# Kernel tuning notes

Measured on AMD Instinct MI355X. Metric: run time of the kernel, lower is better.

The kernel has to match this reference:

```python
import jax, jax.numpy as jnp
import numpy as np
import math

B, S, D, H = 2, 4096, 768, 12
HD = D // H  # head_dim = 64


def setup_inputs() -> dict:
    key = jax.random.key(0)
    ks = jax.random.split(key, 12)
    scale = 1.0 / math.sqrt(D)
    inp = {
        "query": jax.random.normal(ks[0], (B, S, D), jnp.float32),
        "key_": jax.random.normal(ks[1], (B, S, D), jnp.float32),
        "value": jax.random.normal(ks[2], (B, S, D), jnp.float32),
        # causal mask: masked_fill where mask == 0
        "mask": jnp.tril(jnp.ones((S, S), jnp.int32))[None, None, :, :],
        "Wq": jax.random.normal(ks[3], (D, D), jnp.float32) * scale,
        "bq": jax.random.normal(ks[4], (D,), jnp.float32) * scale,
        "Wk": jax.random.normal(ks[5], (D, D), jnp.float32) * scale,
        "bk": jax.random.normal(ks[6], (D,), jnp.float32) * scale,
        "Wv": jax.random.normal(ks[7], (D, D), jnp.float32) * scale,
        "bv": jax.random.normal(ks[8], (D,), jnp.float32) * scale,
        "Wo": jax.random.normal(ks[9], (D, D), jnp.float32) * scale,
        "bo": jax.random.normal(ks[10], (D,), jnp.float32) * scale,
    }
    return inp


def reference(query, key_, value, mask, Wq, bq, Wk, bk, Wv, bv, Wo, bo):
    b, s, d = query.shape
    # Linear: x @ W.T + b (torch convention), split heads -> [B, H, S, HD]
    q = (query @ Wq.T + bq).reshape(b, s, H, HD).transpose(0, 2, 1, 3)
    k = (key_ @ Wk.T + bk).reshape(b, s, H, HD).transpose(0, 2, 1, 3)
    v = (value @ Wv.T + bv).reshape(b, s, H, HD).transpose(0, 2, 1, 3)
    # explicit [B, H, S, S] scores as in the source module
    scores = jnp.einsum("bhqd,bhkd->bhqk", q, k) / math.sqrt(HD)
    scores = jnp.where(mask == 0, -jnp.inf, scores)
    attn = jax.nn.softmax(scores, axis=-1)  # dropout p=0.0 -> identity
    out = jnp.einsum("bhqk,bhkd->bhqd", attn, v)
    out = out.transpose(0, 2, 1, 3).reshape(b, s, d)
    return out @ Wo.T + bo
```

## Files before the change

kernel.cpp:

```cpp
#include <hip/hip_runtime.h>

#define Sq 4096
#define Dm 768
#define Hh 12
#define KD 768

typedef short short8 __attribute__((ext_vector_type(8)));
typedef float f32x4 __attribute__((ext_vector_type(4)));
typedef unsigned short bf_t;

__device__ inline bf_t f2bf(float f) {
    unsigned int u = __builtin_bit_cast(unsigned int, f);
    u += 0x7fffu + ((u >> 16) & 1u);
    return (bf_t)(u >> 16);
}

__device__ inline unsigned int pk2bf(float a, float b) {
    unsigned int ua = __builtin_bit_cast(unsigned int, a) + 0x8000u;
    unsigned int ub = __builtin_bit_cast(unsigned int, b) + 0x8000u;
    return __builtin_amdgcn_perm(ub, ua, 0x07060302);
}

__device__ inline float fexp2(float x) {
#if __has_builtin(__builtin_amdgcn_exp2f)
    return __builtin_amdgcn_exp2f(x);
#else
    return exp2f(x);
#endif
}

__device__ inline void gl_lds16(const void* g, void* l) {
    __builtin_amdgcn_global_load_lds(
        (const __attribute__((address_space(1))) unsigned int*)g,
        (__attribute__((address_space(3))) unsigned int*)l, 16, 0, 0);
}

struct CvtJobs { const float* s[8]; bf_t* d[8]; int n[8]; };

__global__ __launch_bounds__(256) void cvt(CvtJobs jobs) {
    const float* s = jobs.s[blockIdx.z];
    bf_t* d = jobs.d[blockIdx.z];
    int n = jobs.n[blockIdx.z];
    int i = (blockIdx.x * 256 + threadIdx.x) * 8;
    if (i < n) {
        float4 a = *(const float4*)(s + i);
        float4 b = *(const float4*)(s + i + 4);
        short8 p;
        p[0] = (short)f2bf(a.x); p[1] = (short)f2bf(a.y);
        p[2] = (short)f2bf(a.z); p[3] = (short)f2bf(a.w);
        p[4] = (short)f2bf(b.x); p[5] = (short)f2bf(b.y);
        p[6] = (short)f2bf(b.z); p[7] = (short)f2bf(b.w);
        *(short8*)(d + i) = p;
    }
}

struct GemmJob {
    const bf_t* __restrict__ A; const bf_t* __restrict__ Bm;
    const float* __restrict__ bias; void* __restrict__ out;
    int mode; float scale;
};
struct GemmJobs { GemmJob j[3]; };

__global__ __launch_bounds__(256) void gemm_k(GemmJobs jobs) {
    const GemmJob J = jobs.j[blockIdx.z];
    __shared__ bf_t As[128 * 64];
    __shared__ bf_t Bs[128 * 64];
    const int lane = threadIdx.x & 63, wv = threadIdx.x >> 6;
    const int l16 = lane & 15, quad = lane >> 4;
    const int wm = wv >> 1, wn = wv & 1;
    int m0, n0;
    if (J.mode == 1) { m0 = blockIdx.y * 128; n0 = blockIdx.x * 128; }
    else             { m0 = blockIdx.x * 128; n0 = blockIdx.y * 128; }

    f32x4 acc[4][4] = {};

    for (int kk = 0; kk < KD; kk += 64) {
#pragma unroll
        for (int it = 0; it < 4; ++it) {
            int p0 = it * 256 + wv * 64;
            int p = p0 + lane;
            int row = p >> 3;
            int c = (p & 7) ^ (row & 7);
            gl_lds16(J.A + (size_t)(m0 + row) * KD + kk + c * 8, As + p0 * 8);
            gl_lds16(J.Bm + (size_t)(n0 + row) * KD + kk + c * 8, Bs + p0 * 8);
        }
        __syncthreads();
#pragma unroll
        for (int ks = 0; ks < 2; ++ks) {
            short8 a[4], b[4];
#pragma unroll
            for (int i = 0; i < 4; ++i) {
                int row = wm * 64 + i * 16 + l16;
                int pc = (ks * 4 + quad) ^ (row & 7);
                a[i] = *(const short8*)&As[row * 64 + pc * 8];
            }
#pragma unroll
            for (int j = 0; j < 4; ++j) {
                int row = wn * 64 + j * 16 + l16;
                int pc = (ks * 4 + quad) ^ (row & 7);
                b[j] = *(const short8*)&Bs[row * 64 + pc * 8];
            }
#pragma unroll
            for (int i = 0; i < 4; ++i)
#pragma unroll
                for (int j = 0; j < 4; ++j)
                    acc[i][j] = __builtin_amdgcn_mfma_f32_16x16x32_bf16(a[i], b[j], acc[i][j], 0, 0, 0);
        }
        __syncthreads();
    }

#pragma unroll
    for (int i = 0; i < 4; ++i) {
#pragma unroll
        for (int j = 0; j < 4; ++j) {
            int grow = m0 + wm * 64 + i * 16 + quad * 4;
            int gcol = n0 + wn * 64 + j * 16 + l16;
            if (J.mode == 0) {
                float bv = J.bias[gcol];
                int h = gcol >> 6, hd = gcol & 63;
                bf_t* dst = (bf_t*)J.out;
#pragma unroll
                for (int r = 0; r < 4; ++r) {
                    int row = grow + r;
                    int bI = row >> 12, s = row & 4095;
                    dst[(((size_t)(bI * Hh + h) * Sq + s) << 6) + hd] =
                        f2bf((acc[i][j][r] + bv) * J.scale);
                }
            } else if (J.mode == 3) {
                float bv = J.bias[gcol];
                int hh = gcol >> 6, hd = gcol & 63;
                int h2 = hd >> 5, rem = hd & 31, qd = rem >> 3, j2 = rem & 7;
                bf_t* dst = (bf_t*)J.out;
#pragma unroll
                for (int r = 0; r < 4; ++r) {
                    int row = grow + r;
                    int bI = row >> 12, s = row & 4095;
                    int kt2 = s >> 6, rr = s & 63;
                    int g2 = rr >> 5, r5 = rr & 31;
                    int a2 = r5 >> 3, s22 = (r5 >> 2) & 1, b2 = r5 & 3;
                    int lane2 = qd * 16 + (4 * a2 + b2);
                    dst[(size_t)(bI * Hh + hh) * Sq * 64 +
                        kt2 * 4096 + (2 * g2 + s22) * 1024 + h2 * 512 + lane2 * 8 + j2] =
                        f2bf(acc[i][j][r] + bv);
                }
            } else if (J.mode == 1) {
                bf_t* dst = (bf_t*)J.out;
                int t = gcol, bI = t >> 12, s = t & 4095;
                int kt2 = s >> 6, rr = s & 63;
                int g2 = rr >> 5, qd = (rr & 31) >> 3, j2 = rr & 7;
#pragma unroll
                for (int r = 0; r < 4; ++r) {
                    int f = grow + r;
                    int hh = f >> 6, hd = f & 63;
                    int ot = hd >> 4, l16v = hd & 15;
                    int lane2 = qd * 16 + l16v;
                    dst[(size_t)(bI * Hh + hh) * Sq * 64 +
                        kt2 * 4096 + (g2 * 4 + ot) * 512 + lane2 * 8 + j2] =
                        f2bf(acc[i][j][r] + J.bias[f]);
                }
            } else {
                float bv = J.bias[gcol];
                float* dst = (float*)J.out;
#pragma unroll
                for (int r = 0; r < 4; ++r)
                    dst[(size_t)(grow + r) * Dm + gcol] = acc[i][j][r] + bv;
            }
        }
    }
}

#define SHIFT 18.0f
#define NQ 4

__global__ __launch_bounds__(256) void attn(const bf_t* __restrict__ Q,
                                            const bf_t* __restrict__ K,
                                            const bf_t* __restrict__ VT,
                                            bf_t* __restrict__ O) {
    const int id = blockIdx.x + 24 * blockIdx.y;
    const int xcd = id & 7, slot = id >> 3;
    const int bh = xcd * 3 + slot % 3;
    const int qt = 31 - slot / 3;
    const int lane = threadIdx.x & 63, wv = threadIdx.x >> 6;
    const int rg = wv & 1, ksp = wv >> 1;
    const int l16 = lane & 15, quad = lane >> 4;
    const int b = bh / Hh, h = bh % Hh;
    const size_t base = (size_t)bh * Sq * 64;
    const int q0 = qt * 128 + rg * 64;

    __shared__ float ocomb[2][64][68];
    __shared__ float lcomb[2][64];

    const bf_t* __restrict__ Kb = K + base;
    const bf_t* __restrict__ Vb = VT + base;

    short8 qf[NQ][2];
#pragma unroll
    for (int i = 0; i < NQ; ++i) {
        const bf_t* qp = Q + base + (size_t)(q0 + i * 16 + l16) * 64 + quad * 8;
        qf[i][0] = *(const short8*)qp;
        qf[i][1] = *(const short8*)(qp + 32);
    }

    f32x4 oacc[NQ][4] = {};
    f32x4 lsum[NQ] = {};

    const int nkt = (q0 >> 6) + 1;
    const int hsp = (nkt + 1) >> 1;
    const int kt0 = ksp ? hsp : 0;
    const int kt1 = ksp ? nkt : hsp;

    short8 ones32;
#pragma unroll
    for (int j = 0; j < 8; ++j) ones32[j] = (short)0x3F80;

    short8 kf[4][2];
    short8 vfr[4][2];

    int ko = kt0 * 4096 + lane * 8;
    int vo = kt0 * 4096 + lane * 8;

#define LOAD_K()                                                             \
    {                                                                        \
        _Pragma("unroll")                                                    \
        for (int t = 0; t < 4; ++t) {                                        \
            kf[t][0] = *(const short8*)(Kb + ko + t * 1024);                 \
            kf[t][1] = *(const short8*)(Kb + ko + t * 1024 + 512);           \
        }                                                                    \
    }
#define LOAD_V()                                                             \
    {                                                                        \
        _Pragma("unroll")                                                    \
        for (int ot = 0; ot < 4; ++ot)                                       \
            _Pragma("unroll")                                                \
            for (int g = 0; g < 2; ++g)                                      \
                vfr[ot][g] = *(const short8*)(Vb + vo + (g * 4 + ot) * 512); \
    }

    if (kt0 < kt1) { LOAD_K(); LOAD_V(); }

    for (int kt = kt0; kt < kt1; ++kt) {
        const int kv0 = kt * 64;
        const bool more = (kt + 1 < kt1);
#pragma unroll
        for (int i = 0; i < NQ; ++i) {
            f32x4 st[4];
#pragma unroll
            for (int t = 0; t < 4; ++t) {
                f32x4 z = {-SHIFT, -SHIFT, -SHIFT, -SHIFT};
                z = __builtin_amdgcn_mfma_f32_16x16x32_bf16(kf[t][0], qf[i][0], z, 0, 0, 0);
                st[t] = __builtin_amdgcn_mfma_f32_16x16x32_bf16(kf[t][1], qf[i][1], z, 0, 0, 0);
            }
            if (i == NQ - 1) { ko += 4096; if (more) LOAD_K(); }

            alignas(16) unsigned int pkd[4][2];
            const bool need_mask = (kv0 + 63 > q0 + i * 16);
#pragma unroll
            for (int t = 0; t < 4; ++t) {
                int g = t >> 1, s = t & 1;
                f32x4 sv = st[t];
                if (need_mask) {
                    int qrow = q0 + i * 16 + l16;
                    int kb2 = kv0 + 32 * g + 8 * quad + 4 * s;
#pragma unroll
                    for (int r = 0; r < 4; ++r)
                        if (kb2 + r > qrow) sv[r] = -1e30f;
                }
                pkd[t][0] = pk2bf(fexp2(sv[0]), fexp2(sv[1]));
                pkd[t][1] = pk2bf(fexp2(sv[2]), fexp2(sv[3]));
            }
#pragma unroll
            for (int g = 0; g < 2; ++g) {
                short8 pf = *(const short8*)&pkd[2 * g][0];
                lsum[i] = __builtin_amdgcn_mfma_f32_16x16x32_bf16(ones32, pf, lsum[i], 0, 0, 0);
#pragma unroll
                for (int ot = 0; ot < 4; ++ot)
                    oacc[i][ot] = __builtin_amdgcn_mfma_f32_16x16x32_bf16(vfr[ot][g], pf, oacc[i][ot], 0, 0, 0);
            }
        }
        vo += 4096;
        if (more) LOAD_V();
    }
#undef LOAD_K
#undef LOAD_V

    if (ksp) {
#pragma unroll
        for (int i = 0; i < NQ; ++i) {
            int row = i * 16 + l16;
#pragma unroll
            for (int ot = 0; ot < 4; ++ot)
                *(f32x4*)&ocomb[rg][row][ot * 16 + quad * 4] = oacc[i][ot];
            if (quad == 0) lcomb[rg][row] = lsum[i][0];
        }
    }
    __syncthreads();
    if (!ksp) {
#pragma unroll
        for (int i = 0; i < NQ; ++i) {
            int row = i * 16 + l16;
            float ls = lsum[i][0] + lcomb[rg][row];
            float inv = 1.0f / ls;
            int srow = q0 + row;
            bf_t* orow = O + (size_t)(b * Sq + srow) * Dm + h * 64;
#pragma unroll
            for (int ot = 0; ot < 4; ++ot) {
                f32x4 oc = *(const f32x4*)&ocomb[rg][row][ot * 16 + quad * 4];
                uint2 pk;
                pk.x = pk2bf((oacc[i][ot][0] + oc[0]) * inv, (oacc[i][ot][1] + oc[1]) * inv);
                pk.y = pk2bf((oacc[i][ot][2] + oc[2]) * inv, (oacc[i][ot][3] + oc[3]) * inv);
                *(uint2*)(orow + ot * 16 + quad * 4) = pk;
            }
        }
    }
}

extern "C" void kernel_launch(void* const* d_in, const int* in_sizes, int n_in,
                              void* d_out, int out_size, void* d_ws, size_t ws_size,
                              hipStream_t stream) {
    const float* q  = (const float*)d_in[0];
    const float* k  = (const float*)d_in[1];
    const float* v  = (const float*)d_in[2];
    const float* Wq = (const float*)d_in[4];  const float* bq = (const float*)d_in[5];
    const float* Wk = (const float*)d_in[6];  const float* bk = (const float*)d_in[7];
    const float* Wv = (const float*)d_in[8];  const float* bv = (const float*)d_in[9];
    const float* Wo = (const float*)d_in[10]; const float* bo = (const float*)d_in[11];
    float* out = (float*)d_out;

    const float QSCALE = 0.125f * 1.44269504f;

    const size_t NTOK = (size_t)2 * Sq * Dm;
    const size_t NW   = (size_t)Dm * Dm;
    dim3 b256(256);

    const size_t need_main = (6 * NTOK + 4 * NW) * 2;

    if (ws_size >= need_main) {
        bf_t* qb  = (bf_t*)d_ws;
        bf_t* kb  = qb + NTOK;
        bf_t* vb  = kb + NTOK;
        bf_t* xq  = vb + NTOK;
        bf_t* xk  = xq + NTOK;
        bf_t* xv  = xk + NTOK;
        bf_t* wqb = xv + NTOK;
        bf_t* wkb = wqb + NW;
        bf_t* wvb = wkb + NW;
        bf_t* wob = wvb + NW;
        bf_t* ob  = xq;

        CvtJobs cj = {{q, k, v, Wq, Wk, Wv, Wo, q},
                      {xq, xk, xv, wqb, wkb, wvb, wob, xq},
                      {(int)NTOK, (int)NTOK, (int)NTOK,
                       (int)NW, (int)NW, (int)NW, (int)NW, 0}};
        cvt<<<dim3(3072, 1, 7), b256, 0, stream>>>(cj);

        GemmJobs gp;
        gp.j[0] = {xq,  wqb, bq, qb, 0, QSCALE};
        gp.j[1] = {xk,  wkb, bk, kb, 3, 1.0f};
        gp.j[2] = {wvb, xv,  bv, vb, 1, 1.0f};
        gemm_k<<<dim3(64, 6, 3), b256, 0, stream>>>(gp);

        attn<<<dim3(2 * Hh, Sq / 128), b256, 0, stream>>>(qb, kb, vb, ob);

        GemmJobs go;
        go.j[0] = {ob, wob, bo, out, 2, 1.0f};
        go.j[1] = go.j[0]; go.j[2] = go.j[0];
        gemm_k<<<dim3(64, 6, 1), b256, 0, stream>>>(go);
    } else {
        bf_t* qb  = (bf_t*)d_ws;
        bf_t* kb  = qb + NTOK;
        bf_t* vb  = kb + NTOK;
        bf_t* ob  = vb + NTOK;
        bf_t* xc  = ob + NTOK;
        bf_t* wqb = xc + NTOK;
        bf_t* wkb = wqb + NW;
        bf_t* wvb = wkb + NW;
        bf_t* wob = wvb + NW;

        CvtJobs cw = {{Wq, Wk, Wv, Wo, Wq, Wq, Wq, Wq},
                      {wqb, wkb, wvb, wob, wqb, wqb, wqb, wqb},
                      {(int)NW, (int)NW, (int)NW, (int)NW, 0, 0, 0, 0}};
        cvt<<<dim3(288, 1, 4), b256, 0, stream>>>(cw);

        GemmJobs gj;
        CvtJobs c1 = {{q}, {xc}, {(int)NTOK}};
        cvt<<<dim3(3072, 1, 1), b256, 0, stream>>>(c1);
        gj.j[0] = {xc, wqb, bq, qb, 0, QSCALE}; gj.j[1] = gj.j[0]; gj.j[2] = gj.j[0];
        gemm_k<<<dim3(64, 6, 1), b256, 0, stream>>>(gj);

        CvtJobs c2 = {{k}, {xc}, {(int)NTOK}};
        cvt<<<dim3(3072, 1, 1), b256, 0, stream>>>(c2);
        gj.j[0] = {xc, wkb, bk, kb, 3, 1.0f}; gj.j[1] = gj.j[0]; gj.j[2] = gj.j[0];
        gemm_k<<<dim3(64, 6, 1), b256, 0, stream>>>(gj);

        CvtJobs c3 = {{v}, {xc}, {(int)NTOK}};
        cvt<<<dim3(3072, 1, 1), b256, 0, stream>>>(c3);
        gj.j[0] = {wvb, xc, bv, vb, 1, 1.0f}; gj.j[1] = gj.j[0]; gj.j[2] = gj.j[0];
        gemm_k<<<dim3(64, 6, 1), b256, 0, stream>>>(gj);

        attn<<<dim3(2 * Hh, Sq / 128), b256, 0, stream>>>(qb, kb, vb, ob);

        gj.j[0] = {ob, wob, bo, out, 2, 1.0f}; gj.j[1] = gj.j[0]; gj.j[2] = gj.j[0];
        gemm_k<<<dim3(64, 6, 1), b256, 0, stream>>>(gj);
    }
}
```

Baseline: 356.4 us.

## Fuse fp32-to-bf16 activation conversion into QKV projection GEMM loads

The QKV GEMM now reads fp32 activations directly, converts them to bf16 in registers and stores them to LDS, which removes the separate conversion pass and its intermediate buffers. The V projection no longer uses swapped operands; a new output mode writes the transposed V layout from a normal token-by-feature tile. The A-operand load becomes synchronous register loads plus LDS stores instead of direct global-to-LDS copies, so latency hiding in the main loop may suffer. The workspace-size fallback path is dropped.

```diff
diff --git a/kernel.cpp b/kernel.cpp
--- a/kernel.cpp
+++ b/kernel.cpp
@@ -55,9 +55,9 @@
 }
 
 struct GemmJob {
-    const bf_t* __restrict__ A; const bf_t* __restrict__ Bm;
+    const void* __restrict__ A; const bf_t* __restrict__ Bm;
     const float* __restrict__ bias; void* __restrict__ out;
-    int mode; float scale;
+    int mode; float scale; int a32;
 };
 struct GemmJobs { GemmJob j[3]; };
 
@@ -68,21 +68,41 @@
     const int lane = threadIdx.x & 63, wv = threadIdx.x >> 6;
     const int l16 = lane & 15, quad = lane >> 4;
     const int wm = wv >> 1, wn = wv & 1;
-    int m0, n0;
-    if (J.mode == 1) { m0 = blockIdx.y * 128; n0 = blockIdx.x * 128; }
-    else             { m0 = blockIdx.x * 128; n0 = blockIdx.y * 128; }
+    const int m0 = blockIdx.x * 128, n0 = blockIdx.y * 128;
 
     f32x4 acc[4][4] = {};
 
     for (int kk = 0; kk < KD; kk += 64) {
-#pragma unroll
-        for (int it = 0; it < 4; ++it) {
-            int p0 = it * 256 + wv * 64;
-            int p = p0 + lane;
-            int row = p >> 3;
-            int c = (p & 7) ^ (row & 7);
-            gl_lds16(J.A + (size_t)(m0 + row) * KD + kk + c * 8, As + p0 * 8);
-            gl_lds16(J.Bm + (size_t)(n0 + row) * KD + kk + c * 8, Bs + p0 * 8);
+        if (J.a32) {
+            const float* A32 = (const float*)J.A;
+#pragma unroll
+            for (int it = 0; it < 4; ++it) {
+                int p0 = it * 256 + wv * 64;
+                int p = p0 + lane;
+                int row = p >> 3;
+                int c = (p & 7) ^ (row & 7);
+                const float* src = A32 + (size_t)(m0 + row) * KD + kk + c * 8;
+                float4 a0 = *(const float4*)src;
+                float4 a1 = *(const float4*)(src + 4);
+                short8 pp;
+                pp[0] = (short)f2bf(a0.x); pp[1] = (short)f2bf(a0.y);
+                pp[2] = (short)f2bf(a0.z); pp[3] = (short)f2bf(a0.w);
+                pp[4] = (short)f2bf(a1.x); pp[5] = (short)f2bf(a1.y);
+                pp[6] = (short)f2bf(a1.z); pp[7] = (short)f2bf(a1.w);
+                *(short8*)&As[p * 8] = pp;
+                gl_lds16(J.Bm + (size_t)(n0 + row) * KD + kk + c * 8, Bs + p0 * 8);
+            }
+        } else {
+            const bf_t* Ab = (const bf_t*)J.A;
+#pragma unroll
+            for (int it = 0; it < 4; ++it) {
+                int p0 = it * 256 + wv * 64;
+                int p = p0 + lane;
+                int row = p >> 3;
+                int c = (p & 7) ^ (row & 7);
+                gl_lds16(Ab + (size_t)(m0 + row) * KD + kk + c * 8, As + p0 * 8);
+                gl_lds16(J.Bm + (size_t)(n0 + row) * KD + kk + c * 8, Bs + p0 * 8);
+            }
         }
         __syncthreads();
 #pragma unroll
@@ -143,20 +163,21 @@
                         kt2 * 4096 + (2 * g2 + s22) * 1024 + h2 * 512 + lane2 * 8 + j2] =
                         f2bf(acc[i][j][r] + bv);
                 }
-            } else if (J.mode == 1) {
+            } else if (J.mode == 4) {
+                float bv = J.bias[gcol];
+                int hh = gcol >> 6, hd = gcol & 63;
+                int ot = hd >> 4, l16v = hd & 15;
                 bf_t* dst = (bf_t*)J.out;
-                int t = gcol, bI = t >> 12, s = t & 4095;
-                int kt2 = s >> 6, rr = s & 63;
-                int g2 = rr >> 5, qd = (rr & 31) >> 3, j2 = rr & 7;
 #pragma unroll
                 for (int r = 0; r < 4; ++r) {
-                    int f = grow + r;
-                    int hh = f >> 6, hd = f & 63;
-                    int ot = hd >> 4, l16v = hd & 15;
+                    int row = grow + r;
+                    int bI = row >> 12, s = row & 4095;
+                    int kt2 = s >> 6, rr = s & 63;
+                    int g2 = rr >> 5, qd = (rr & 31) >> 3, j2 = rr & 7;
                     int lane2 = qd * 16 + l16v;
                     dst[(size_t)(bI * Hh + hh) * Sq * 64 +
                         kt2 * 4096 + (g2 * 4 + ot) * 512 + lane2 * 8 + j2] =
-                        f2bf(acc[i][j][r] + J.bias[f]);
+                        f2bf(acc[i][j][r] + bv);
                 }
             } else {
                 float bv = J.bias[gcol];
@@ -332,74 +353,30 @@
     const size_t NW   = (size_t)Dm * Dm;
     dim3 b256(256);
 
-    const size_t need_main = (6 * NTOK + 4 * NW) * 2;
-
-    if (ws_size >= need_main) {
-        bf_t* qb  = (bf_t*)d_ws;
-        bf_t* kb  = qb + NTOK;
-        bf_t* vb  = kb + NTOK;
-        bf_t* xq  = vb + NTOK;
-        bf_t* xk  = xq + NTOK;
-        bf_t* xv  = xk + NTOK;
-        bf_t* wqb = xv + NTOK;
-        bf_t* wkb = wqb + NW;
-        bf_t* wvb = wkb + NW;
-        bf_t* wob = wvb + NW;
-        bf_t* ob  = xq;
-
-        CvtJobs cj = {{q, k, v, Wq, Wk, Wv, Wo, q},
-                      {xq, xk, xv, wqb, wkb, wvb, wob, xq},
-                      {(int)NTOK, (int)NTOK, (int)NTOK,
-                       (int)NW, (int)NW, (int)NW, (int)NW, 0}};
-        cvt<<<dim3(3072, 1, 7), b256, 0, stream>>>(cj);
-
-        GemmJobs gp;
-        gp.j[0] = {xq,  wqb, bq, qb, 0, QSCALE};
-        gp.j[1] = {xk,  wkb, bk, kb, 3, 1.0f};
-        gp.j[2] = {wvb, xv,  bv, vb, 1, 1.0f};
-        gemm_k<<<dim3(64, 6, 3), b256, 0, stream>>>(gp);
-
-        attn<<<dim3(2 * Hh, Sq / 128), b256, 0, stream>>>(qb, kb, vb, ob);
-
-        GemmJobs go;
-        go.j[0] = {ob, wob, bo, out, 2, 1.0f};
-        go.j[1] = go.j[0]; go.j[2] = go.j[0];
-        gemm_k<<<dim3(64, 6, 1), b256, 0, stream>>>(go);
-    } else {
-        bf_t* qb  = (bf_t*)d_ws;
-        bf_t* kb  = qb + NTOK;
-        bf_t* vb  = kb + NTOK;
-        bf_t* ob  = vb + NTOK;
-        bf_t* xc  = ob + NTOK;
-        bf_t* wqb = xc + NTOK;
-        bf_t* wkb = wqb + NW;
-        bf_t* wvb = wkb + NW;
-        bf_t* wob = wvb + NW;
-
-        CvtJobs cw = {{Wq, Wk, Wv, Wo, Wq, Wq, Wq, Wq},
-                      {wqb, wkb, wvb, wob, wqb, wqb, wqb, wqb},
-                      {(int)NW, (int)NW, (int)NW, (int)NW, 0, 0, 0, 0}};
-        cvt<<<dim3(288, 1, 4), b256, 0, stream>>>(cw);
-
-        GemmJobs gj;
-        CvtJobs c1 = {{q}, {xc}, {(int)NTOK}};
-        cvt<<<dim3(3072, 1, 1), b256, 0, stream>>>(c1);
-        gj.j[0] = {xc, wqb, bq, qb, 0, QSCALE}; gj.j[1] = gj.j[0]; gj.j[2] = gj.j[0];
-        gemm_k<<<dim3(64, 6, 1), b256, 0, stream>>>(gj);
-
-        CvtJobs c2 = {{k}, {xc}, {(int)NTOK}};
-        cvt<<<dim3(3072, 1, 1), b256, 0, stream>>>(c2);
-        gj.j[0] = {xc, wkb, bk, kb, 3, 1.0f}; gj.j[1] = gj.j[0]; gj.j[2] = gj.j[0];
-        gemm_k<<<dim3(64, 6, 1), b256, 0, stream>>>(gj);
-
-        CvtJobs c3 = {{v}, {xc}, {(int)NTOK}};
-        cvt<<<dim3(3072, 1, 1), b256, 0, stream>>>(c3);
-        gj.j[0] = {wvb, xc, bv, vb, 1, 1.0f}; gj.j[1] = gj.j[0]; gj.j[2] = gj.j[0];
-        gemm_k<<<dim3(64, 6, 1), b256, 0, stream>>>(gj);
-
-        attn<<<dim3(2 * Hh, Sq / 128), b256, 0, stream>>>(qb, kb, vb, ob);
-
-        gj.j[0] = {ob, wob, bo, out, 2, 1.0f}; gj.j[1] = gj.j[0]; gj.j[2] = gj.j[0];
-        gemm_k<<<dim3(64, 6, 1), b256, 0, stream>>>(gj);
-    }
-}
+    bf_t* qb  = (bf_t*)d_ws;
+    bf_t* kb  = qb + NTOK;
+    bf_t* vb  = kb + NTOK;
+    bf_t* ob  = vb + NTOK;
+    bf_t* wqb = ob + NTOK;
+    bf_t* wkb = wqb + NW;
+    bf_t* wvb = wkb + NW;
+    bf_t* wob = wvb + NW;
+
+    CvtJobs cw = {{Wq, Wk, Wv, Wo, Wq, Wq, Wq, Wq},
+                  {wqb, wkb, wvb, wob, wqb, wqb, wqb, wqb},
+                  {(int)NW, (int)NW, (int)NW, (int)NW, 0, 0, 0, 0}};
+    cvt<<<dim3(288, 1, 4), b256, 0, stream>>>(cw);
+
+    GemmJobs gp;
+    gp.j[0] = {q, wqb, bq, qb, 0, QSCALE, 1};
+    gp.j[1] = {k, wkb, bk, kb, 3, 1.0f, 1};
+    gp.j[2] = {v, wvb, bv, vb, 4, 1.0f, 1};
+    gemm_k<<<dim3(64, 6, 3), b256, 0, stream>>>(gp);
+
+    attn<<<dim3(2 * Hh, Sq / 128), b256, 0, stream>>>(qb, kb, vb, ob);
+
+    GemmJobs go;
+    go.j[0] = {ob, wob, bo, out, 2, 1.0f, 0};
+    go.j[1] = go.j[0]; go.j[2] = go.j[0];
+    gemm_k<<<dim3(64, 6, 1), b256, 0, stream>>>(go);
+}
```

Measured after the change: 358.8 us. No clear change (+0.7%).
